# Kernel optimization log

Measured on AMD Instinct MI355X. Metric: run time of the kernel, lower is better.

## Reference

```python
import jax, jax.numpy as jnp
import numpy as np

BBOX_MIN = jnp.array([0.6, 0.6, 0.2], dtype=jnp.float32)
BBOX_MAX = jnp.array([-0.8, -1.2, -0.2], dtype=jnp.float32)
# level resolutions: floor(16 * (4096/16)**(l/15)) for l in 0..4
RES = [16, 23, 33, 48, 70]
OFFS = np.cumsum([0] + [(r + 1) ** 3 for r in RES]).tolist()  # dense grids fit in 2^21 hashmap


def _encode(x, table):
    # x: [N,3] in [0,1]; table: [533601, 2] concatenated dense per-level grids
    feats = []
    for l, r in enumerate(RES):
        g = r + 1  # grid points per axis
        pos = x * r
        p0 = jnp.clip(jnp.floor(pos), 0.0, r - 1)
        f = pos - p0  # trilinear weights, [N,3]
        p0 = p0.astype(jnp.int32)
        acc = jnp.zeros((x.shape[0], 2), dtype=table.dtype)
        for dx in (0, 1):
            for dy in (0, 1):
                for dz in (0, 1):
                    idx = ((p0[:, 0] + dx) * g + (p0[:, 1] + dy)) * g + (p0[:, 2] + dz) + OFFS[l]
                    wx = f[:, 0] if dx else 1.0 - f[:, 0]
                    wy = f[:, 1] if dy else 1.0 - f[:, 1]
                    wz = f[:, 2] if dz else 1.0 - f[:, 2]
                    acc = acc + (wx * wy * wz)[:, None] * table[idx]
        feats.append(acc)
    return jnp.concatenate(feats, axis=-1)  # [N, 10]


def setup_inputs() -> dict:
    key = jax.random.key(0)
    ks = jax.random.split(key, 5)
    T = OFFS[-1]  # 533601
    return {
        "texc": jax.random.uniform(ks[0], (2048, 2048, 3), dtype=jnp.float32),
        "table": jax.random.normal(ks[1], (T, 2), dtype=jnp.float32) * 1e-4,
        "W0": jax.random.normal(ks[2], (32, 10), dtype=jnp.float32) * (2.0 / 10) ** 0.5,
        "W1": jax.random.normal(ks[3], (32, 32), dtype=jnp.float32) * (2.0 / 32) ** 0.5,
        "W2": jax.random.normal(ks[4], (3, 32), dtype=jnp.float32) * (2.0 / 32) ** 0.5,
        "min_val": jnp.zeros((3,), jnp.float32),
        "max_val": jnp.ones((3,), jnp.float32),
        "frame_id": 0,
    }


def reference(texc, table, W0, W1, W2, min_val, max_val, frame_id):
    x = texc.reshape(-1, 3)
    # coordinate normalization into [0,1] with hardcoded bbox (as in source)
    x = jnp.clip((x - BBOX_MIN) / (BBOX_MAX - BBOX_MIN), 0.0, 1.0)
    p = _encode(x, table)              # [N, 10]
    h = jax.nn.relu(p @ W0.T)          # [N, 32]
    h = jax.nn.relu(h @ W1.T)          # [N, 32]
    o = h @ W2.T                       # [N, 3]
    o = jax.nn.sigmoid(o) * (max_val - min_val) + min_val
    return o.reshape(*texc.shape[:-1], 3)
```

## Files before the change

### kernel.cpp

```cpp
#include <hip/hip_runtime.h>
#include <hip/hip_bf16.h>
#include <math.h>


#if defined(__has_builtin)
#  if __has_builtin(__builtin_amdgcn_cvt_pk_f32_fp8) && __has_builtin(__builtin_amdgcn_cvt_pk_fp8_f32)
#    define HAVE_FP8 1
#  else
#    define HAVE_FP8 0
#  endif
#else
#  define HAVE_FP8 0
#endif

namespace {

typedef __attribute__((ext_vector_type(8)))  short short8;
typedef __attribute__((ext_vector_type(16))) float f32x16;
typedef __attribute__((ext_vector_type(2)))  float f32x2;
typedef __attribute__((ext_vector_type(4), aligned(8)))  float f32x4a;
typedef __attribute__((ext_vector_type(4), aligned(16))) unsigned int u32x4;

union S8 { short8 v; int d[4]; };

#define SWAP32(a, b) asm volatile("v_permlane32_swap_b32 %0, %1" : "+v"(a), "+v"(b))

constexpr int RES0 = 16, RES1 = 23, RES2 = 33, RES3 = 48, RES4 = 70;
constexpr int TOFF0 = 0, TOFF1 = 4913, TOFF2 = 18737, TOFF3 = 58041, TOFF4 = 175690;
constexpr int COFF0 = 0;
constexpr int COFF1 = COFF0 + RES0*RES0*RES0;
constexpr int COFF2 = COFF1 + RES1*RES1*RES1;
constexpr int COFF3 = COFF2 + RES2*RES2*RES2;
constexpr int COFF4 = COFF3 + RES3*RES3*RES3;
constexpr int NCELL = COFF4 + RES4*RES4*RES4;
constexpr size_t WS_NEED_FP8  = (size_t)NCELL * 16u;
constexpr size_t WS_NEED_BF16 = (size_t)NCELL * 32u;

constexpr float FP8_SCALE = 8192.0f;
constexpr float FP8_INV   = 1.0f / 8192.0f;

constexpr int PPT = 4;

__device__ __forceinline__ int cvt_pk(float lo, float hi) {
    int d;
    asm("v_cvt_pk_bf16_f32 %0, %1, %2" : "=v"(d) : "v"(lo), "v"(hi));
    return d;
}

__device__ __forceinline__ short8 pack8(float4 a, float4 b) {
    S8 u;
    u.d[0] = cvt_pk(a.x, a.y);
    u.d[1] = cvt_pk(a.z, a.w);
    u.d[2] = cvt_pk(b.x, b.y);
    u.d[3] = cvt_pk(b.z, b.w);
    return u.v;
}

__device__ __forceinline__ float clamp01(float v) {
    return fminf(fmaxf(v, 0.0f), 1.0f);
}

__device__ __forceinline__ f32x2 up2(unsigned int u) {
    f32x2 r;
    r[0] = __uint_as_float(u << 16);
    r[1] = __uint_as_float(u & 0xffff0000u);
    return r;
}

__device__ __forceinline__ f32x2 lerp2(f32x2 a, f32x2 b, float t) {
    return a + (b - a) * t;
}

__device__ __forceinline__ void marshal_h(const f32x16& acc, short8& k0, short8& k1) {
    const f32x2* a2 = reinterpret_cast<const f32x2*>(&acc);
    const f32x2 z2 = {0.0f, 0.0f};
    int q[8];
    #pragma unroll
    for (int j = 0; j < 8; ++j) {
        f32x2 m = __builtin_elementwise_max(a2[j], z2);
        q[j] = cvt_pk(m[0], m[1]);
    }
    int a0 = q[0], b0 = q[2]; SWAP32(a0, b0);
    int a1 = q[1], b1 = q[3]; SWAP32(a1, b1);
    int a2_ = q[4], b2 = q[6]; SWAP32(a2_, b2);
    int a3 = q[5], b3 = q[7]; SWAP32(a3, b3);
    S8 u0; u0.d[0] = a0;  u0.d[1] = a1; u0.d[2] = b0; u0.d[3] = b1; k0 = u0.v;
    S8 u1; u1.d[0] = a2_; u1.d[1] = a3; u1.d[2] = b2; u1.d[3] = b3; k1 = u1.v;
}

template<int R, int TOFF, int COFF>
__device__ __forceinline__ void cell_coords(int ci, int& base) {
    constexpr int G = R + 1;
    int lc = ci - COFF;
    int cz = lc % R;
    int t  = lc / R;
    int cy = t % R;
    int cx = t / R;
    base = (cx * G + cy) * G + cz + TOFF;
}

#if HAVE_FP8
template<int R, int TOFF, int COFF>
__device__ __forceinline__ void prep_level_fp8(int ci, const float2* __restrict__ tab2,
                                               unsigned int* __restrict__ ws)
{
    constexpr int G = R + 1;
    int base; cell_coords<R, TOFF, COFF>(ci, base);

    f32x4a q00 = *reinterpret_cast<const f32x4a*>(tab2 + base);
    f32x4a q01 = *reinterpret_cast<const f32x4a*>(tab2 + base + G);
    f32x4a q10 = *reinterpret_cast<const f32x4a*>(tab2 + base + G*G);
    f32x4a q11 = *reinterpret_cast<const f32x4a*>(tab2 + base + G*G + G);

    u32x4 c;
    int w;
    w = __builtin_amdgcn_cvt_pk_fp8_f32(q00[0]*FP8_SCALE, q00[1]*FP8_SCALE, 0, false);
    w = __builtin_amdgcn_cvt_pk_fp8_f32(q00[2]*FP8_SCALE, q00[3]*FP8_SCALE, w, true);
    c.x = (unsigned int)w;
    w = __builtin_amdgcn_cvt_pk_fp8_f32(q01[0]*FP8_SCALE, q01[1]*FP8_SCALE, 0, false);
    w = __builtin_amdgcn_cvt_pk_fp8_f32(q01[2]*FP8_SCALE, q01[3]*FP8_SCALE, w, true);
    c.y = (unsigned int)w;
    w = __builtin_amdgcn_cvt_pk_fp8_f32(q10[0]*FP8_SCALE, q10[1]*FP8_SCALE, 0, false);
    w = __builtin_amdgcn_cvt_pk_fp8_f32(q10[2]*FP8_SCALE, q10[3]*FP8_SCALE, w, true);
    c.z = (unsigned int)w;
    w = __builtin_amdgcn_cvt_pk_fp8_f32(q11[0]*FP8_SCALE, q11[1]*FP8_SCALE, 0, false);
    w = __builtin_amdgcn_cvt_pk_fp8_f32(q11[2]*FP8_SCALE, q11[3]*FP8_SCALE, w, true);
    c.w = (unsigned int)w;

    __builtin_nontemporal_store(c, reinterpret_cast<u32x4*>(ws + (size_t)ci * 4));
}

__global__ __launch_bounds__(256) void prep_kernel_fp8(
    const float* __restrict__ table, unsigned int* __restrict__ ws)
{
    int ci = blockIdx.x * blockDim.x + threadIdx.x;
    const float2* tab2 = reinterpret_cast<const float2*>(table);
    if      (ci < COFF1) prep_level_fp8<RES0, TOFF0, COFF0>(ci, tab2, ws);
    else if (ci < COFF2) prep_level_fp8<RES1, TOFF1, COFF1>(ci, tab2, ws);
    else if (ci < COFF3) prep_level_fp8<RES2, TOFF2, COFF2>(ci, tab2, ws);
    else if (ci < COFF4) prep_level_fp8<RES3, TOFF3, COFF3>(ci, tab2, ws);
    else if (ci < NCELL) prep_level_fp8<RES4, TOFF4, COFF4>(ci, tab2, ws);
}
#endif

template<int R, int TOFF, int COFF>
__device__ __forceinline__ void prep_level_bf16(int ci, const float2* __restrict__ tab2,
                                                unsigned int* __restrict__ ws)
{
    constexpr int G = R + 1;
    int base; cell_coords<R, TOFF, COFF>(ci, base);

    f32x4a q00 = *reinterpret_cast<const f32x4a*>(tab2 + base);
    f32x4a q01 = *reinterpret_cast<const f32x4a*>(tab2 + base + G);
    f32x4a q10 = *reinterpret_cast<const f32x4a*>(tab2 + base + G*G);
    f32x4a q11 = *reinterpret_cast<const f32x4a*>(tab2 + base + G*G + G);

    u32x4 lo, hi;
    lo.x = (unsigned int)cvt_pk(q00[0], q00[1]);
    lo.y = (unsigned int)cvt_pk(q00[2], q00[3]);
    lo.z = (unsigned int)cvt_pk(q01[0], q01[1]);
    lo.w = (unsigned int)cvt_pk(q01[2], q01[3]);
    hi.x = (unsigned int)cvt_pk(q10[0], q10[1]);
    hi.y = (unsigned int)cvt_pk(q10[2], q10[3]);
    hi.z = (unsigned int)cvt_pk(q11[0], q11[1]);
    hi.w = (unsigned int)cvt_pk(q11[2], q11[3]);

    u32x4* dst = reinterpret_cast<u32x4*>(ws + (size_t)ci * 8);
    __builtin_nontemporal_store(lo, dst);
    __builtin_nontemporal_store(hi, dst + 1);
}

__global__ __launch_bounds__(256) void prep_kernel_bf16(
    const float* __restrict__ table, unsigned int* __restrict__ ws)
{
    int ci = blockIdx.x * blockDim.x + threadIdx.x;
    const float2* tab2 = reinterpret_cast<const float2*>(table);
    if      (ci < COFF1) prep_level_bf16<RES0, TOFF0, COFF0>(ci, tab2, ws);
    else if (ci < COFF2) prep_level_bf16<RES1, TOFF1, COFF1>(ci, tab2, ws);
    else if (ci < COFF3) prep_level_bf16<RES2, TOFF2, COFF2>(ci, tab2, ws);
    else if (ci < COFF4) prep_level_bf16<RES3, TOFF3, COFF3>(ci, tab2, ws);
    else if (ci < NCELL) prep_level_bf16<RES4, TOFF4, COFF4>(ci, tab2, ws);
}

template<int MODE>
__device__ __forceinline__ void encode(float x, float y, float z,
    const void* __restrict__ cells, const float2* __restrict__ tab2,
    float* __restrict__ pf)
{
    const int RESL[5]  = {RES0, RES1, RES2, RES3, RES4};
    const int TOFFL[5] = {TOFF0, TOFF1, TOFF2, TOFF3, TOFF4};
    const int COFFL[5] = {COFF0, COFF1, COFF2, COFF3, COFF4};

    #pragma unroll
    for (int l = 0; l < 5; ++l) {
        const int r = RESL[l];
        const int g = r + 1;
        const float rf = (float)r;
        float px = x * rf, py = y * rf, pz = z * rf;
        float fx = fminf(floorf(px), rf - 1.0f);
        float fy = fminf(floorf(py), rf - 1.0f);
        float fz = fminf(floorf(pz), rf - 1.0f);
        float tx = px - fx, ty = py - fy, tz = pz - fz;
        int ix = (int)fx & 127, iy = (int)fy & 127, iz = (int)fz & 127;

        if constexpr (MODE == 3) {
#if HAVE_FP8
            int ci = (ix * r + iy) * r + iz + COFFL[l];
            u32x4 c = *reinterpret_cast<const u32x4*>(
                (const unsigned int*)cells + (size_t)ci * 4);
            f32x2 c000 = __builtin_amdgcn_cvt_pk_f32_fp8(c.x, false);
            f32x2 c001 = __builtin_amdgcn_cvt_pk_f32_fp8(c.x, true);
            f32x2 c010 = __builtin_amdgcn_cvt_pk_f32_fp8(c.y, false);
            f32x2 c011 = __builtin_amdgcn_cvt_pk_f32_fp8(c.y, true);
            f32x2 c100 = __builtin_amdgcn_cvt_pk_f32_fp8(c.z, false);
            f32x2 c101 = __builtin_amdgcn_cvt_pk_f32_fp8(c.z, true);
            f32x2 c110 = __builtin_amdgcn_cvt_pk_f32_fp8(c.w, false);
            f32x2 c111 = __builtin_amdgcn_cvt_pk_f32_fp8(c.w, true);
            f32x2 z00 = lerp2(c000, c001, tz);
            f32x2 z01 = lerp2(c010, c011, tz);
            f32x2 z10 = lerp2(c100, c101, tz);
            f32x2 z11 = lerp2(c110, c111, tz);
            f32x2 y0 = lerp2(z00, z01, ty);
            f32x2 y1 = lerp2(z10, z11, ty);
            f32x2 f  = lerp2(y0, y1, tx);
            pf[2*l+0] = f[0] * FP8_INV;
            pf[2*l+1] = f[1] * FP8_INV;
#endif
        } else if constexpr (MODE == 1) {
            int ci = (ix * r + iy) * r + iz + COFFL[l];
            const u32x4* cp = reinterpret_cast<const u32x4*>(
                (const unsigned int*)cells + (size_t)ci * 8);
            u32x4 lo = cp[0];
            u32x4 hi = cp[1];
            f32x2 z00 = lerp2(up2(lo.x), up2(lo.y), tz);
            f32x2 z01 = lerp2(up2(lo.z), up2(lo.w), tz);
            f32x2 z10 = lerp2(up2(hi.x), up2(hi.y), tz);
            f32x2 z11 = lerp2(up2(hi.z), up2(hi.w), tz);
            f32x2 y0 = lerp2(z00, z01, ty);
            f32x2 y1 = lerp2(z10, z11, ty);
            f32x2 f  = lerp2(y0, y1, tx);
            pf[2*l+0] = f[0];
            pf[2*l+1] = f[1];
        } else {
            const int gg = g * g;
            int base = (ix * g + iy) * g + iz + TOFFL[l];
            f32x4a q00 = *reinterpret_cast<const f32x4a*>(tab2 + base);
            f32x4a q01 = *reinterpret_cast<const f32x4a*>(tab2 + base + g);
            f32x4a q10 = *reinterpret_cast<const f32x4a*>(tab2 + base + gg);
            f32x4a q11 = *reinterpret_cast<const f32x4a*>(tab2 + base + gg + g);
            f32x2 z00 = lerp2((f32x2){q00[0], q00[1]}, (f32x2){q00[2], q00[3]}, tz);
            f32x2 z01 = lerp2((f32x2){q01[0], q01[1]}, (f32x2){q01[2], q01[3]}, tz);
            f32x2 z10 = lerp2((f32x2){q10[0], q10[1]}, (f32x2){q10[2], q10[3]}, tz);
            f32x2 z11 = lerp2((f32x2){q11[0], q11[1]}, (f32x2){q11[2], q11[3]}, tz);
            f32x2 y0 = lerp2(z00, z01, ty);
            f32x2 y1 = lerp2(z10, z11, ty);
            f32x2 f  = lerp2(y0, y1, tx);
            pf[2*l+0] = f[0];
            pf[2*l+1] = f[1];
        }
    }
}

__device__ __forceinline__ void run_mlp(const float* __restrict__ pf,
    short8 w0f, short8 w1f0, short8 w1f1, short8 w2f0, short8 w2f1,
    int lane, float* __restrict__ v)
{
    int pk0 = cvt_pk(pf[0], pf[1]);
    int pk1 = cvt_pk(pf[2], pf[3]);
    int pk2 = cvt_pk(pf[4], pf[5]);
    int pk3 = cvt_pk(pf[6], pf[7]);
    int pk4 = cvt_pk(pf[8], pf[9]);

    int n1d0 = pk0, n2d0 = pk4; SWAP32(n1d0, n2d0);
    int n1d1 = pk1, n2d1 = 0;   SWAP32(n1d1, n2d1);
    int n1d2 = pk2, n2d2 = 0;   SWAP32(n1d2, n2d2);
    int n1d3 = pk3, n2d3 = 0;   SWAP32(n1d3, n2d3);
    S8 ub1; ub1.d[0]=n1d0; ub1.d[1]=n1d1; ub1.d[2]=n1d2; ub1.d[3]=n1d3;
    S8 ub2; ub2.d[0]=n2d0; ub2.d[1]=n2d1; ub2.d[2]=n2d2; ub2.d[3]=n2d3;

    const f32x16 zero16 = {0.f,0.f,0.f,0.f,0.f,0.f,0.f,0.f,
                           0.f,0.f,0.f,0.f,0.f,0.f,0.f,0.f};

    f32x16 h0a = __builtin_amdgcn_mfma_f32_32x32x16_bf16(w0f, ub1.v, zero16, 0, 0, 0);
    f32x16 h0b = __builtin_amdgcn_mfma_f32_32x32x16_bf16(w0f, ub2.v, zero16, 0, 0, 0);

    short8 h0a_k0, h0a_k1, h0b_k0, h0b_k1;
    marshal_h(h0a, h0a_k0, h0a_k1);
    marshal_h(h0b, h0b_k0, h0b_k1);

    f32x16 h1a = __builtin_amdgcn_mfma_f32_32x32x16_bf16(w1f0, h0a_k0, zero16, 0, 0, 0);
    h1a = __builtin_amdgcn_mfma_f32_32x32x16_bf16(w1f1, h0a_k1, h1a, 0, 0, 0);
    f32x16 h1b = __builtin_amdgcn_mfma_f32_32x32x16_bf16(w1f0, h0b_k0, zero16, 0, 0, 0);
    h1b = __builtin_amdgcn_mfma_f32_32x32x16_bf16(w1f1, h0b_k1, h1b, 0, 0, 0);

    short8 h1a_k0, h1a_k1, h1b_k0, h1b_k1;
    marshal_h(h1a, h1a_k0, h1a_k1);
    marshal_h(h1b, h1b_k0, h1b_k1);

    f32x16 oa = __builtin_amdgcn_mfma_f32_32x32x16_bf16(w2f0, h1a_k0, zero16, 0, 0, 0);
    oa = __builtin_amdgcn_mfma_f32_32x32x16_bf16(w2f1, h1a_k1, oa, 0, 0, 0);
    f32x16 ob = __builtin_amdgcn_mfma_f32_32x32x16_bf16(w2f0, h1b_k0, zero16, 0, 0, 0);
    ob = __builtin_amdgcn_mfma_f32_32x32x16_bf16(w2f1, h1b_k1, ob, 0, 0, 0);

    #pragma unroll
    for (int j = 0; j < 3; ++j) {
        float t0 = ob[j], t1 = ob[j];
        SWAP32(t0, t1);
        v[j] = (lane < 32) ? oa[j] : t0;
    }
}

template<int MODE>
__global__ __launch_bounds__(512) void mlptex_kernel(
    const float* __restrict__ texc,
    const float* __restrict__ table,
    const void* __restrict__ cells,
    const float* __restrict__ W0,
    const float* __restrict__ W1,
    const float* __restrict__ W2,
    const float* __restrict__ minv,
    const float* __restrict__ maxv,
    float* __restrict__ out,
    int N)
{
    const int H   = N / PPT;
    const int tid = blockIdx.x * blockDim.x + threadIdx.x;
    const int lane = threadIdx.x & 63;
    const int pt0 = min(tid, H - 1);
    const bool live = (tid < H);

    const int row = lane & 31;
    const int kb  = lane >> 5;

    short8 w0f, w1f0, w1f1;
    {
        const float* p0 = W0 + row * 10;
        float4 a, b;
        if (kb == 0) {
            float2 f0 = *(const float2*)(p0 + 0);
            float2 f1 = *(const float2*)(p0 + 2);
            float2 f2 = *(const float2*)(p0 + 4);
            float2 f3 = *(const float2*)(p0 + 6);
            a = make_float4(f0.x, f0.y, f1.x, f1.y);
            b = make_float4(f2.x, f2.y, f3.x, f3.y);
        } else {
            float2 f4 = *(const float2*)(p0 + 8);
            a = make_float4(f4.x, f4.y, 0.f, 0.f);
            b = make_float4(0.f, 0.f, 0.f, 0.f);
        }
        w0f = pack8(a, b);

        const float* p1 = W1 + row * 32 + kb * 8;
        w1f0 = pack8(*(const float4*)(p1),      *(const float4*)(p1 + 4));
        w1f1 = pack8(*(const float4*)(p1 + 16), *(const float4*)(p1 + 20));
    }
    short8 w2f0 = {0,0,0,0,0,0,0,0}, w2f1 = {0,0,0,0,0,0,0,0};
    if (row < 3) {
        const float* p2 = W2 + row * 32 + kb * 8;
        w2f0 = pack8(*(const float4*)(p2),      *(const float4*)(p2 + 4));
        w2f1 = pack8(*(const float4*)(p2 + 16), *(const float4*)(p2 + 20));
    }

    float xs[PPT], ys[PPT], zs[PPT];
    #pragma unroll
    for (int k = 0; k < PPT; ++k) {
        const float* tp = texc + 3 * (pt0 + k * H);
        float x = __builtin_nontemporal_load(tp + 0);
        float y = __builtin_nontemporal_load(tp + 1);
        float z = __builtin_nontemporal_load(tp + 2);
        xs[k] = clamp01((x - 0.6f) * (-1.0f/1.4f));
        ys[k] = clamp01((y - 0.6f) * (-1.0f/1.8f));
        zs[k] = clamp01((z - 0.2f) * (-1.0f/0.4f));
    }

    const float2* tab2 = reinterpret_cast<const float2*>(table);

    float pf[PPT][10];
    #pragma unroll
    for (int k = 0; k < PPT; ++k)
        encode<MODE>(xs[k], ys[k], zs[k], cells, tab2, pf[k]);

    float v[PPT][3];
    #pragma unroll
    for (int k = 0; k < PPT; ++k)
        run_mlp(pf[k], w0f, w1f0, w1f1, w2f0, w2f1, lane, v[k]);

    float mn[3] = {minv[0], minv[1], minv[2]};
    float sc[3] = {maxv[0] - minv[0], maxv[1] - minv[1], maxv[2] - minv[2]};

    if (live) {
        #pragma unroll
        for (int k = 0; k < PPT; ++k) {
            float* op = out + 3 * (pt0 + k * H);
            #pragma unroll
            for (int j = 0; j < 3; ++j) {
                float s = 1.0f / (1.0f + __expf(-v[k][j]));
                __builtin_nontemporal_store(fmaf(s, sc[j], mn[j]), op + j);
            }
        }
    }
}

}

extern "C" void kernel_launch(void* const* d_in, const int* in_sizes, int n_in,
                              void* d_out, int out_size, void* d_ws, size_t ws_size,
                              hipStream_t stream) {
    const float* texc  = (const float*)d_in[0];
    const float* table = (const float*)d_in[1];
    const float* W0    = (const float*)d_in[2];
    const float* W1    = (const float*)d_in[3];
    const float* W2    = (const float*)d_in[4];
    const float* minv  = (const float*)d_in[5];
    const float* maxv  = (const float*)d_in[6];
    float* out = (float*)d_out;

    const int N = in_sizes[0] / 3;
    const int threads = 512;
    const int blocks = ((N / PPT) + threads - 1) / threads;
    const int pblocks = (NCELL + 255) / 256;

#if HAVE_FP8
    if (ws_size >= WS_NEED_FP8) {
        unsigned int* cells = (unsigned int*)d_ws;
        prep_kernel_fp8<<<pblocks, 256, 0, stream>>>(table, cells);
        mlptex_kernel<3><<<blocks, threads, 0, stream>>>(
            texc, table, cells, W0, W1, W2, minv, maxv, out, N);
        return;
    }
#endif
    if (ws_size >= WS_NEED_BF16) {
        unsigned int* cells = (unsigned int*)d_ws;
        prep_kernel_bf16<<<pblocks, 256, 0, stream>>>(table, cells);
        mlptex_kernel<1><<<blocks, threads, 0, stream>>>(
            texc, table, cells, W0, W1, W2, minv, maxv, out, N);
    } else {
        mlptex_kernel<0><<<blocks, threads, 0, stream>>>(
            texc, table, nullptr, W0, W1, W2, minv, maxv, out, N);
    }
}
```

Baseline: 196.1 us.

## Batch FP8 cell gathers across points per level and fold FP8 scale into W0

Result: no change. 200.0 us (+2.0%).

```diff
diff --git a/kernel.cpp b/kernel.cpp
--- a/kernel.cpp
+++ b/kernel.cpp
@@ -203,30 +203,7 @@
         float tx = px - fx, ty = py - fy, tz = pz - fz;
         int ix = (int)fx & 127, iy = (int)fy & 127, iz = (int)fz & 127;
 
-        if constexpr (MODE == 3) {
-#if HAVE_FP8
-            int ci = (ix * r + iy) * r + iz + COFFL[l];
-            u32x4 c = *reinterpret_cast<const u32x4*>(
-                (const unsigned int*)cells + (size_t)ci * 4);
-            f32x2 c000 = __builtin_amdgcn_cvt_pk_f32_fp8(c.x, false);
-            f32x2 c001 = __builtin_amdgcn_cvt_pk_f32_fp8(c.x, true);
-            f32x2 c010 = __builtin_amdgcn_cvt_pk_f32_fp8(c.y, false);
-            f32x2 c011 = __builtin_amdgcn_cvt_pk_f32_fp8(c.y, true);
-            f32x2 c100 = __builtin_amdgcn_cvt_pk_f32_fp8(c.z, false);
-            f32x2 c101 = __builtin_amdgcn_cvt_pk_f32_fp8(c.z, true);
-            f32x2 c110 = __builtin_amdgcn_cvt_pk_f32_fp8(c.w, false);
-            f32x2 c111 = __builtin_amdgcn_cvt_pk_f32_fp8(c.w, true);
-            f32x2 z00 = lerp2(c000, c001, tz);
-            f32x2 z01 = lerp2(c010, c011, tz);
-            f32x2 z10 = lerp2(c100, c101, tz);
-            f32x2 z11 = lerp2(c110, c111, tz);
-            f32x2 y0 = lerp2(z00, z01, ty);
-            f32x2 y1 = lerp2(z10, z11, ty);
-            f32x2 f  = lerp2(y0, y1, tx);
-            pf[2*l+0] = f[0] * FP8_INV;
-            pf[2*l+1] = f[1] * FP8_INV;
-#endif
-        } else if constexpr (MODE == 1) {
+        if constexpr (MODE == 1) {
             int ci = (ix * r + iy) * r + iz + COFFL[l];
             const u32x4* cp = reinterpret_cast<const u32x4*>(
                 (const unsigned int*)cells + (size_t)ci * 8);
@@ -311,7 +288,7 @@
 }
 
 template<int MODE>
-__global__ __launch_bounds__(512) void mlptex_kernel(
+__global__ __launch_bounds__(256, 4) void mlptex_kernel(
     const float* __restrict__ texc,
     const float* __restrict__ table,
     const void* __restrict__ cells,
@@ -332,6 +309,8 @@
     const int row = lane & 31;
     const int kb  = lane >> 5;
 
+    const float w0s = (MODE == 3) ? FP8_INV : 1.0f;
+
     short8 w0f, w1f0, w1f1;
     {
         const float* p0 = W0 + row * 10;
@@ -341,11 +320,11 @@
             float2 f1 = *(const float2*)(p0 + 2);
             float2 f2 = *(const float2*)(p0 + 4);
             float2 f3 = *(const float2*)(p0 + 6);
-            a = make_float4(f0.x, f0.y, f1.x, f1.y);
-            b = make_float4(f2.x, f2.y, f3.x, f3.y);
+            a = make_float4(f0.x*w0s, f0.y*w0s, f1.x*w0s, f1.y*w0s);
+            b = make_float4(f2.x*w0s, f2.y*w0s, f3.x*w0s, f3.y*w0s);
         } else {
             float2 f4 = *(const float2*)(p0 + 8);
-            a = make_float4(f4.x, f4.y, 0.f, 0.f);
+            a = make_float4(f4.x*w0s, f4.y*w0s, 0.f, 0.f);
             b = make_float4(0.f, 0.f, 0.f, 0.f);
         }
         w0f = pack8(a, b);
@@ -376,9 +355,55 @@
     const float2* tab2 = reinterpret_cast<const float2*>(table);
 
     float pf[PPT][10];
-    #pragma unroll
-    for (int k = 0; k < PPT; ++k)
-        encode<MODE>(xs[k], ys[k], zs[k], cells, tab2, pf[k]);
+    if constexpr (MODE == 3) {
+#if HAVE_FP8
+        const int RESL[5]  = {RES0, RES1, RES2, RES3, RES4};
+        const int COFFL[5] = {COFF0, COFF1, COFF2, COFF3, COFF4};
+        const unsigned int* cw = (const unsigned int*)cells;
+        #pragma unroll
+        for (int l = 0; l < 5; ++l) {
+            const int r = RESL[l];
+            const float rf = (float)r;
+            float tx[PPT], ty[PPT], tz[PPT];
+            u32x4 c[PPT];
+            #pragma unroll
+            for (int k = 0; k < PPT; ++k) {
+                float px = xs[k]*rf, py = ys[k]*rf, pz = zs[k]*rf;
+                float fx = fminf(floorf(px), rf - 1.0f);
+                float fy = fminf(floorf(py), rf - 1.0f);
+                float fz = fminf(floorf(pz), rf - 1.0f);
+                tx[k] = px - fx; ty[k] = py - fy; tz[k] = pz - fz;
+                int ix = (int)fx & 127, iy = (int)fy & 127, iz = (int)fz & 127;
+                int ci = (ix * r + iy) * r + iz + COFFL[l];
+                c[k] = *reinterpret_cast<const u32x4*>(cw + (size_t)ci * 4);
+            }
+            #pragma unroll
+            for (int k = 0; k < PPT; ++k) {
+                f32x2 c000 = __builtin_amdgcn_cvt_pk_f32_fp8(c[k].x, false);
+                f32x2 c001 = __builtin_amdgcn_cvt_pk_f32_fp8(c[k].x, true);
+                f32x2 c010 = __builtin_amdgcn_cvt_pk_f32_fp8(c[k].y, false);
+                f32x2 c011 = __builtin_amdgcn_cvt_pk_f32_fp8(c[k].y, true);
+                f32x2 c100 = __builtin_amdgcn_cvt_pk_f32_fp8(c[k].z, false);
+                f32x2 c101 = __builtin_amdgcn_cvt_pk_f32_fp8(c[k].z, true);
+                f32x2 c110 = __builtin_amdgcn_cvt_pk_f32_fp8(c[k].w, false);
+                f32x2 c111 = __builtin_amdgcn_cvt_pk_f32_fp8(c[k].w, true);
+                f32x2 z00 = lerp2(c000, c001, tz[k]);
+                f32x2 z01 = lerp2(c010, c011, tz[k]);
+                f32x2 z10 = lerp2(c100, c101, tz[k]);
+                f32x2 z11 = lerp2(c110, c111, tz[k]);
+                f32x2 y0 = lerp2(z00, z01, ty[k]);
+                f32x2 y1 = lerp2(z10, z11, ty[k]);
+                f32x2 f  = lerp2(y0, y1, tx[k]);
+                pf[k][2*l+0] = f[0];
+                pf[k][2*l+1] = f[1];
+            }
+        }
+#endif
+    } else {
+        #pragma unroll
+        for (int k = 0; k < PPT; ++k)
+            encode<MODE>(xs[k], ys[k], zs[k], cells, tab2, pf[k]);
+    }
 
     float v[PPT][3];
     #pragma unroll
@@ -416,7 +441,7 @@
     float* out = (float*)d_out;
 
     const int N = in_sizes[0] / 3;
-    const int threads = 512;
+    const int threads = 256;
     const int blocks = ((N / PPT) + threads - 1) / threads;
     const int pblocks = (NCELL + 255) / 256;
 
```

## Cut register pressure by packing features early and serializing MLP halves

Applied to the files above, without the earlier changes.

Result: slower. 210.1 us (+7.2%).

```diff
diff --git a/kernel.cpp b/kernel.cpp
--- a/kernel.cpp
+++ b/kernel.cpp
@@ -185,7 +185,7 @@
 template<int MODE>
 __device__ __forceinline__ void encode(float x, float y, float z,
     const void* __restrict__ cells, const float2* __restrict__ tab2,
-    float* __restrict__ pf)
+    int* __restrict__ pk)
 {
     const int RESL[5]  = {RES0, RES1, RES2, RES3, RES4};
     const int TOFFL[5] = {TOFF0, TOFF1, TOFF2, TOFF3, TOFF4};
@@ -203,6 +203,7 @@
         float tx = px - fx, ty = py - fy, tz = pz - fz;
         int ix = (int)fx & 127, iy = (int)fy & 127, iz = (int)fz & 127;
 
+        f32x2 f;
         if constexpr (MODE == 3) {
 #if HAVE_FP8
             int ci = (ix * r + iy) * r + iz + COFFL[l];
@@ -222,9 +223,7 @@
             f32x2 z11 = lerp2(c110, c111, tz);
             f32x2 y0 = lerp2(z00, z01, ty);
             f32x2 y1 = lerp2(z10, z11, ty);
-            f32x2 f  = lerp2(y0, y1, tx);
-            pf[2*l+0] = f[0] * FP8_INV;
-            pf[2*l+1] = f[1] * FP8_INV;
+            f = lerp2(y0, y1, tx);
 #endif
         } else if constexpr (MODE == 1) {
             int ci = (ix * r + iy) * r + iz + COFFL[l];
@@ -238,9 +237,7 @@
             f32x2 z11 = lerp2(up2(hi.z), up2(hi.w), tz);
             f32x2 y0 = lerp2(z00, z01, ty);
             f32x2 y1 = lerp2(z10, z11, ty);
-            f32x2 f  = lerp2(y0, y1, tx);
-            pf[2*l+0] = f[0];
-            pf[2*l+1] = f[1];
+            f = lerp2(y0, y1, tx);
         } else {
             const int gg = g * g;
             int base = (ix * g + iy) * g + iz + TOFFL[l];
@@ -254,59 +251,51 @@
             f32x2 z11 = lerp2((f32x2){q11[0], q11[1]}, (f32x2){q11[2], q11[3]}, tz);
             f32x2 y0 = lerp2(z00, z01, ty);
             f32x2 y1 = lerp2(z10, z11, ty);
-            f32x2 f  = lerp2(y0, y1, tx);
-            pf[2*l+0] = f[0];
-            pf[2*l+1] = f[1];
+            f = lerp2(y0, y1, tx);
         }
-    }
-}
-
-__device__ __forceinline__ void run_mlp(const float* __restrict__ pf,
+        pk[l] = cvt_pk(f[0], f[1]);
+    }
+}
+
+__device__ __forceinline__ void run_mlp(const int* __restrict__ pk,
     short8 w0f, short8 w1f0, short8 w1f1, short8 w2f0, short8 w2f1,
     int lane, float* __restrict__ v)
 {
-    int pk0 = cvt_pk(pf[0], pf[1]);
-    int pk1 = cvt_pk(pf[2], pf[3]);
-    int pk2 = cvt_pk(pf[4], pf[5]);
-    int pk3 = cvt_pk(pf[6], pf[7]);
-    int pk4 = cvt_pk(pf[8], pf[9]);
-
-    int n1d0 = pk0, n2d0 = pk4; SWAP32(n1d0, n2d0);
-    int n1d1 = pk1, n2d1 = 0;   SWAP32(n1d1, n2d1);
-    int n1d2 = pk2, n2d2 = 0;   SWAP32(n1d2, n2d2);
-    int n1d3 = pk3, n2d3 = 0;   SWAP32(n1d3, n2d3);
+    int n1d0 = pk[0], n2d0 = pk[4]; SWAP32(n1d0, n2d0);
+    int n1d1 = pk[1], n2d1 = 0;     SWAP32(n1d1, n2d1);
+    int n1d2 = pk[2], n2d2 = 0;     SWAP32(n1d2, n2d2);
+    int n1d3 = pk[3], n2d3 = 0;     SWAP32(n1d3, n2d3);
     S8 ub1; ub1.d[0]=n1d0; ub1.d[1]=n1d1; ub1.d[2]=n1d2; ub1.d[3]=n1d3;
     S8 ub2; ub2.d[0]=n2d0; ub2.d[1]=n2d1; ub2.d[2]=n2d2; ub2.d[3]=n2d3;
 
     const f32x16 zero16 = {0.f,0.f,0.f,0.f,0.f,0.f,0.f,0.f,
                            0.f,0.f,0.f,0.f,0.f,0.f,0.f,0.f};
-
-    f32x16 h0a = __builtin_amdgcn_mfma_f32_32x32x16_bf16(w0f, ub1.v, zero16, 0, 0, 0);
-    f32x16 h0b = __builtin_amdgcn_mfma_f32_32x32x16_bf16(w0f, ub2.v, zero16, 0, 0, 0);
-
-    short8 h0a_k0, h0a_k1, h0b_k0, h0b_k1;
-    marshal_h(h0a, h0a_k0, h0a_k1);
-    marshal_h(h0b, h0b_k0, h0b_k1);
-
-    f32x16 h1a = __builtin_amdgcn_mfma_f32_32x32x16_bf16(w1f0, h0a_k0, zero16, 0, 0, 0);
-    h1a = __builtin_amdgcn_mfma_f32_32x32x16_bf16(w1f1, h0a_k1, h1a, 0, 0, 0);
-    f32x16 h1b = __builtin_amdgcn_mfma_f32_32x32x16_bf16(w1f0, h0b_k0, zero16, 0, 0, 0);
-    h1b = __builtin_amdgcn_mfma_f32_32x32x16_bf16(w1f1, h0b_k1, h1b, 0, 0, 0);
-
-    short8 h1a_k0, h1a_k1, h1b_k0, h1b_k1;
-    marshal_h(h1a, h1a_k0, h1a_k1);
-    marshal_h(h1b, h1b_k0, h1b_k1);
-
-    f32x16 oa = __builtin_amdgcn_mfma_f32_32x32x16_bf16(w2f0, h1a_k0, zero16, 0, 0, 0);
-    oa = __builtin_amdgcn_mfma_f32_32x32x16_bf16(w2f1, h1a_k1, oa, 0, 0, 0);
-    f32x16 ob = __builtin_amdgcn_mfma_f32_32x32x16_bf16(w2f0, h1b_k0, zero16, 0, 0, 0);
-    ob = __builtin_amdgcn_mfma_f32_32x32x16_bf16(w2f1, h1b_k1, ob, 0, 0, 0);
-
+    short8 m0, m1;
+
+    f32x16 h = __builtin_amdgcn_mfma_f32_32x32x16_bf16(w0f, ub1.v, zero16, 0, 0, 0);
+    marshal_h(h, m0, m1);
+    h = __builtin_amdgcn_mfma_f32_32x32x16_bf16(w1f0, m0, zero16, 0, 0, 0);
+    h = __builtin_amdgcn_mfma_f32_32x32x16_bf16(w1f1, m1, h, 0, 0, 0);
+    marshal_h(h, m0, m1);
+    h = __builtin_amdgcn_mfma_f32_32x32x16_bf16(w2f0, m0, zero16, 0, 0, 0);
+    h = __builtin_amdgcn_mfma_f32_32x32x16_bf16(w2f1, m1, h, 0, 0, 0);
+    float va0 = h[0], va1 = h[1], va2 = h[2];
+
+    h = __builtin_amdgcn_mfma_f32_32x32x16_bf16(w0f, ub2.v, zero16, 0, 0, 0);
+    marshal_h(h, m0, m1);
+    h = __builtin_amdgcn_mfma_f32_32x32x16_bf16(w1f0, m0, zero16, 0, 0, 0);
+    h = __builtin_amdgcn_mfma_f32_32x32x16_bf16(w1f1, m1, h, 0, 0, 0);
+    marshal_h(h, m0, m1);
+    h = __builtin_amdgcn_mfma_f32_32x32x16_bf16(w2f0, m0, zero16, 0, 0, 0);
+    h = __builtin_amdgcn_mfma_f32_32x32x16_bf16(w2f1, m1, h, 0, 0, 0);
+
+    float vb[3] = {h[0], h[1], h[2]};
     #pragma unroll
     for (int j = 0; j < 3; ++j) {
-        float t0 = ob[j], t1 = ob[j];
+        float t0 = vb[j], t1 = vb[j];
         SWAP32(t0, t1);
-        v[j] = (lane < 32) ? oa[j] : t0;
+        float va = (j == 0) ? va0 : (j == 1) ? va1 : va2;
+        v[j] = (lane < 32) ? va : t0;
     }
 }
 
@@ -332,6 +321,8 @@
     const int row = lane & 31;
     const int kb  = lane >> 5;
 
+    const float w0s = (MODE == 3) ? FP8_INV : 1.0f;
+
     short8 w0f, w1f0, w1f1;
     {
         const float* p0 = W0 + row * 10;
@@ -341,11 +332,11 @@
             float2 f1 = *(const float2*)(p0 + 2);
             float2 f2 = *(const float2*)(p0 + 4);
             float2 f3 = *(const float2*)(p0 + 6);
-            a = make_float4(f0.x, f0.y, f1.x, f1.y);
-            b = make_float4(f2.x, f2.y, f3.x, f3.y);
+            a = make_float4(f0.x*w0s, f0.y*w0s, f1.x*w0s, f1.y*w0s);
+            b = make_float4(f2.x*w0s, f2.y*w0s, f3.x*w0s, f3.y*w0s);
         } else {
             float2 f4 = *(const float2*)(p0 + 8);
-            a = make_float4(f4.x, f4.y, 0.f, 0.f);
+            a = make_float4(f4.x*w0s, f4.y*w0s, 0.f, 0.f);
             b = make_float4(0.f, 0.f, 0.f, 0.f);
         }
         w0f = pack8(a, b);
@@ -361,40 +352,33 @@
         w2f1 = pack8(*(const float4*)(p2 + 16), *(const float4*)(p2 + 20));
     }
 
-    float xs[PPT], ys[PPT], zs[PPT];
+    const float2* tab2 = reinterpret_cast<const float2*>(table);
+
+    int pk[PPT][5];
     #pragma unroll
     for (int k = 0; k < PPT; ++k) {
         const float* tp = texc + 3 * (pt0 + k * H);
         float x = __builtin_nontemporal_load(tp + 0);
         float y = __builtin_nontemporal_load(tp + 1);
         float z = __builtin_nontemporal_load(tp + 2);
-        xs[k] = clamp01((x - 0.6f) * (-1.0f/1.4f));
-        ys[k] = clamp01((y - 0.6f) * (-1.0f/1.8f));
-        zs[k] = clamp01((z - 0.2f) * (-1.0f/0.4f));
-    }
-
-    const float2* tab2 = reinterpret_cast<const float2*>(table);
-
-    float pf[PPT][10];
-    #pragma unroll
-    for (int k = 0; k < PPT; ++k)
-        encode<MODE>(xs[k], ys[k], zs[k], cells, tab2, pf[k]);
-
-    float v[PPT][3];
-    #pragma unroll
-    for (int k = 0; k < PPT; ++k)
-        run_mlp(pf[k], w0f, w1f0, w1f1, w2f0, w2f1, lane, v[k]);
+        x = clamp01((x - 0.6f) * (-1.0f/1.4f));
+        y = clamp01((y - 0.6f) * (-1.0f/1.8f));
+        z = clamp01((z - 0.2f) * (-1.0f/0.4f));
+        encode<MODE>(x, y, z, cells, tab2, pk[k]);
+    }
 
     float mn[3] = {minv[0], minv[1], minv[2]};
     float sc[3] = {maxv[0] - minv[0], maxv[1] - minv[1], maxv[2] - minv[2]};
 
-    if (live) {
-        #pragma unroll
-        for (int k = 0; k < PPT; ++k) {
+    #pragma unroll
+    for (int k = 0; k < PPT; ++k) {
+        float v[3];
+        run_mlp(pk[k], w0f, w1f0, w1f1, w2f0, w2f1, lane, v);
+        if (live) {
             float* op = out + 3 * (pt0 + k * H);
             #pragma unroll
             for (int j = 0; j < 3; ++j) {
-                float s = 1.0f / (1.0f + __expf(-v[k][j]));
+                float s = 1.0f / (1.0f + __expf(-v[j]));
                 __builtin_nontemporal_store(fmaf(s, sc[j], mn[j]), op + j);
             }
         }
```
